# Kernel optimization log

Measured on AMD Instinct MI355X. Metric: run time of the kernel, lower is better.

The kernel has to match this reference:

```python
import jax, jax.numpy as jnp
import numpy as np

B, C, H, W = 8, 256, 128, 128


def _bilinear_sample(img, gx, gy):
    """F.grid_sample(bilinear, padding_mode='zeros', align_corners=False).
    img: [B,C,H,W]; gx, gy: [B,H,W] normalized coords in [-1,1].
    Returns [B,C,H,W]."""
    Bi, Ci, Hi, Wi = img.shape
    ix = ((gx + 1.0) * Wi - 1.0) * 0.5  # pixel x coord
    iy = ((gy + 1.0) * Hi - 1.0) * 0.5  # pixel y coord
    ix0 = jnp.floor(ix)
    iy0 = jnp.floor(iy)
    wx1 = ix - ix0
    wy1 = iy - iy0
    bidx = jnp.arange(Bi)[:, None, None]

    def gather(iyf, ixf):
        valid = (ixf >= 0) & (ixf < Wi) & (iyf >= 0) & (iyf < Hi)
        iyc = jnp.clip(iyf, 0, Hi - 1).astype(jnp.int32)
        ixc = jnp.clip(ixf, 0, Wi - 1).astype(jnp.int32)
        v = img[bidx, :, iyc, ixc]  # [B,H,W,C]
        return jnp.where(valid[..., None], v, jnp.zeros((), img.dtype))

    v00 = gather(iy0, ix0)
    v01 = gather(iy0, ix0 + 1)
    v10 = gather(iy0 + 1, ix0)
    v11 = gather(iy0 + 1, ix0 + 1)
    w00 = ((1.0 - wy1) * (1.0 - wx1))[..., None]
    w01 = ((1.0 - wy1) * wx1)[..., None]
    w10 = (wy1 * (1.0 - wx1))[..., None]
    w11 = (wy1 * wx1)[..., None]
    out = v00 * w00 + v01 * w01 + v10 * w10 + v11 * w11  # [B,H,W,C]
    return out.transpose(0, 3, 1, 2)


def setup_inputs() -> dict:
    key = jax.random.key(0)
    ks = jax.random.split(key, 7)
    s = 1.0 / np.sqrt(C)
    return {
        "x": jax.random.normal(ks[0], (B, C, H, W), jnp.float32),
        "w_dw": jax.random.normal(ks[1], (C,), jnp.float32) * s,        # depthwise 1x1, no bias
        "w_off": jax.random.normal(ks[2], (2, C), jnp.float32) * s,     # offset 1x1 conv C->2
        "b_off": jax.random.normal(ks[3], (2,), jnp.float32) * 0.1,
        "w_pc": jax.random.normal(ks[4], (C, C), jnp.float32) * s,      # pointwise 1x1, no bias
        "w_W": jax.random.normal(ks[5], (C, C), jnp.float32) * s,       # residual-merge 1x1 conv
        "b_W": jax.random.normal(ks[6], (C,), jnp.float32) * 0.1,
    }


def reference(x, w_dw, w_off, b_off, w_pc, w_W, b_W):
    # offset = tanh(Conv1x1(x)) -> one shared (dx, dy) field (group == inplanes)
    offset = jnp.tanh(jnp.einsum('oc,bchw->bohw', w_off, x) + b_off[None, :, None, None])
    # depthwise 1x1 conv (bias=False) == per-channel scale
    dw = x * w_dw[None, :, None, None]
    # base normalized grid: X varies along W, Y along H (np.meshgrid convention)
    gx_base = jnp.linspace(-1.0, 1.0, W)[None, None, :]  # [1,1,W]
    gy_base = jnp.linspace(-1.0, 1.0, H)[None, :, None]  # [1,H,1]
    gx = jnp.clip(gx_base + offset[:, 0], -1.0, 1.0)  # [B,H,W]
    gy = jnp.clip(gy_base + offset[:, 1], -1.0, 1.0)
    sampled = _bilinear_sample(dw, gx, gy)             # [B,C,H,W]
    out = jnp.einsum('oc,bchw->bohw', w_pc, sampled)   # pointwise conv
    out = jnp.einsum('oc,bchw->bohw', w_W, out) + b_W[None, :, None, None]
    return out + x
```

## Files before the change

### kernel.cpp

```cpp
#include <hip/hip_runtime.h>
#include <hip/hip_bf16.h>

#define Bn 8
#define Cn 256
#define Hn 128
#define Wn 128
#define HWn (Hn * Wn)

typedef __attribute__((ext_vector_type(8))) short bfrag8;
typedef __attribute__((ext_vector_type(8))) unsigned short u16x8;
typedef __attribute__((ext_vector_type(4))) float f32x4;
typedef __attribute__((ext_vector_type(4))) unsigned int u32x4;

__device__ __forceinline__ float bf2f(unsigned short u) {
    unsigned int v = ((unsigned int)u) << 16;
    return __builtin_bit_cast(float, v);
}
__device__ __forceinline__ unsigned short f2bf(float f) {
    unsigned int u = __builtin_bit_cast(unsigned int, f);
    unsigned int lsb = (u >> 16) & 1u;
    u += 0x7fffu + lsb;
    return (unsigned short)(u >> 16);
}

__device__ __forceinline__ void load_lds16(const void* g, void* l) {
    __builtin_amdgcn_global_load_lds(
        (const __attribute__((address_space(1))) unsigned int*)g,
        (__attribute__((address_space(3))) unsigned int*)l,
        16, 0, 0);
}

__global__ __launch_bounds__(256)
void build_wcomb(const float* __restrict__ w_dw,
                 const float* __restrict__ w_pc,
                 const float* __restrict__ w_W,
                 unsigned short* __restrict__ wfrag) {
    const int o = blockIdx.x;
    const int c = threadIdx.x;
    float acc = 0.f;
#pragma unroll 8
    for (int k = 0; k < Cn; ++k)
        acc = fmaf(w_W[o * Cn + k], w_pc[k * Cn + c], acc);
    const int ob = o >> 4, lr = o & 15;
    const int ks = c >> 5, lg = (c & 31) >> 3, e = c & 7;
    const int lane = (lg << 4) + lr;
    wfrag[((((ob << 3) + ks) << 6) + lane) * 8 + e] = f2bf(acc * w_dw[c]);
}

__global__ __launch_bounds__(256)
void prep_kernel(const float* __restrict__ x,
                 const float* __restrict__ w_off,
                 const float* __restrict__ b_off,
                 unsigned short* __restrict__ x_t,
                 float2* __restrict__ coords) {
    __shared__ __align__(16) char tile[64 * 512];
    __shared__ float partial[4][64][2];
    const int t = threadIdx.x;
    const int lane = t & 63;
    const int wv = t >> 6;
    int blk = blockIdx.x;
    blk = ((blk & 7) << 8) | (blk >> 3);
    const int b = blk >> 8;
    const int p0 = (blk & 255) << 6;
    const float* xp = x + ((size_t)b * Cn) * HWn + p0;

    float s0 = 0.f, s1 = 0.f;
#pragma unroll 8
    for (int i = 0; i < 64; ++i) {
        int c = (wv << 6) + i;
        float v = xp[(size_t)c * HWn + lane];
        s0 = fmaf(v, w_off[c], s0);
        s1 = fmaf(v, w_off[Cn + c], s1);
        int byte = (lane << 9) + (((c << 1)) ^ ((lane & 7) << 4));
        *reinterpret_cast<unsigned short*>(tile + byte) = f2bf(v);
    }
    partial[wv][lane][0] = s0;
    partial[wv][lane][1] = s1;
    __syncthreads();

    if (t < 64) {
        float o0 = partial[0][t][0] + partial[1][t][0] + partial[2][t][0] + partial[3][t][0] + b_off[0];
        float o1 = partial[0][t][1] + partial[1][t][1] + partial[2][t][1] + partial[3][t][1] + b_off[1];
        o0 = tanhf(o0);
        o1 = tanhf(o1);
        int p = p0 + t;
        int yy = p >> 7, xx = p & 127;
        float gx = fminf(fmaxf(-1.f + xx * (2.f / 127.f) + o0, -1.f), 1.f);
        float gy = fminf(fmaxf(-1.f + yy * (2.f / 127.f) + o1, -1.f), 1.f);
        coords[(size_t)b * HWn + p] = make_float2(gx * 64.f + 63.5f, gy * 64.f + 63.5f);
    }

    const int pp = t >> 2, cc = t & 3;
    unsigned short* dst = x_t + ((size_t)(b * HWn + p0 + pp)) * Cn + (cc << 6);
#pragma unroll
    for (int j = 0; j < 8; ++j) {
        int c2 = ((cc << 6) + (j << 3)) << 1;
        int byte = (pp << 9) + (c2 ^ ((pp & 7) << 4));
        *reinterpret_cast<u32x4*>(dst + (j << 3)) = *reinterpret_cast<const u32x4*>(tile + byte);
    }
}

__global__ __launch_bounds__(512, 2)
void main_kernel(const float* __restrict__ x,
                 const float* __restrict__ b_W,
                 const unsigned short* __restrict__ x_t,
                 const float2* __restrict__ coords,
                 const unsigned short* __restrict__ wfrag,
                 float* __restrict__ out) {
    __shared__ __align__(16) char As[4][32 * 512];
    __shared__ __align__(16) float4 wts[32];
    const int t = threadIdx.x;
    const int lane = t & 63;
    const int wid = t >> 6;
    int blk = blockIdx.x;
    blk = ((blk & 7) << 9) | (blk >> 3);
    const int b = blk >> 9;
    const int p0 = (blk & 511) << 5;
    const size_t pixbase = (size_t)b * HWn + p0;
    const unsigned short* xtb = x_t + (size_t)b * HWn * Cn;

    if (t < 32) {
        float2 co = coords[pixbase + t];
        float ix = co.x, iy = co.y;
        float fx = floorf(ix), fy = floorf(iy);
        int ix0 = (int)fx, iy0 = (int)fy;
        float wx1 = ix - fx, wy1 = iy - fy;
        float wx0 = 1.f - wx1, wy0 = 1.f - wy1;
        bool vx0 = (ix0 >= 0) && (ix0 < Wn);
        bool vx1 = (ix0 >= -1) && (ix0 < Wn - 1);
        bool vy0 = (iy0 >= 0) && (iy0 < Hn);
        bool vy1 = (iy0 >= -1) && (iy0 < Hn - 1);
        float4 w;
        w.x = (vy0 && vx0) ? wy0 * wx0 : 0.f;
        w.y = (vy0 && vx1) ? wy0 * wx1 : 0.f;
        w.z = (vy1 && vx0) ? wy1 * wx0 : 0.f;
        w.w = (vy1 && vx1) ? wy1 * wx1 : 0.f;
        wts[t] = w;
    }

    {
        const int hp = lane >> 5;
        const int j = lane & 31;
        float2 co[2];
#pragma unroll
        for (int i = 0; i < 2; ++i)
            co[i] = coords[pixbase + (wid << 2) + (i << 1) + hp];

#pragma unroll
        for (int i = 0; i < 2; ++i) {
            const int p = (wid << 2) + (i << 1);
            const int px = p + hp;
            float ix = co[i].x, iy = co[i].y;
            int ix0 = (int)floorf(ix), iy0 = (int)floorf(iy);
            int cx0 = min(max(ix0, 0), Wn - 1), cx1 = min(max(ix0 + 1, 0), Wn - 1);
            int cy0 = min(max(iy0, 0), Hn - 1), cy1 = min(max(iy0 + 1, 0), Hn - 1);
            const int gch = (j ^ (px & 15)) << 3;
            const unsigned short* s00 = xtb + (size_t)(cy0 * Wn + cx0) * Cn + gch;
            const unsigned short* s01 = xtb + (size_t)(cy0 * Wn + cx1) * Cn + gch;
            const unsigned short* s10 = xtb + (size_t)(cy1 * Wn + cx0) * Cn + gch;
            const unsigned short* s11 = xtb + (size_t)(cy1 * Wn + cx1) * Cn + gch;
            load_lds16(s00, &As[0][p << 9]);
            load_lds16(s01, &As[1][p << 9]);
            load_lds16(s10, &As[2][p << 9]);
            load_lds16(s11, &As[3][p << 9]);
        }
    }
    __syncthreads();

    {
        const int px = t >> 4;
        const float4 w = wts[px];
#pragma unroll
        for (int q = 0; q < 2; ++q) {
            const int kc = (t & 15) + (q << 4);
            const int off = (px << 9) + ((kc ^ (px & 15)) << 4);
            u16x8 c00 = *reinterpret_cast<const u16x8*>(&As[0][off]);
            u16x8 c01 = *reinterpret_cast<const u16x8*>(&As[1][off]);
            u16x8 c10 = *reinterpret_cast<const u16x8*>(&As[2][off]);
            u16x8 c11 = *reinterpret_cast<const u16x8*>(&As[3][off]);
            u16x8 res;
#pragma unroll
            for (int e = 0; e < 8; ++e) {
                float r = w.x * bf2f(c00[e]) + w.y * bf2f(c01[e])
                        + w.z * bf2f(c10[e]) + w.w * bf2f(c11[e]);
                res[e] = f2bf(r);
            }
            *reinterpret_cast<u16x8*>(&As[0][off]) = res;
        }
    }
    __syncthreads();

    const int lr = lane & 15;
    const int lg = lane >> 4;
    f32x4 acc[2][2];
#pragma unroll
    for (int m = 0; m < 2; ++m)
#pragma unroll
        for (int n = 0; n < 2; ++n)
            acc[m][n] = (f32x4){0.f, 0.f, 0.f, 0.f};

#pragma unroll
    for (int ks = 0; ks < 8; ++ks) {
        bfrag8 a[2], bb[2];
        const int kc = (ks << 2) + lg;
#pragma unroll
        for (int n = 0; n < 2; ++n) {
            const int pr = (n << 4) + lr;
            const int off = (pr << 9) + ((kc ^ (pr & 15)) << 4);
            bb[n] = *reinterpret_cast<const bfrag8*>(&As[0][off]);
        }
#pragma unroll
        for (int m = 0; m < 2; ++m) {
            const int ob = (wid << 1) + m;
            const unsigned short* src = wfrag + ((((ob << 3) + ks) << 6) + lane) * 8;
            a[m] = *reinterpret_cast<const bfrag8*>(src);
        }
#pragma unroll
        for (int m = 0; m < 2; ++m)
#pragma unroll
            for (int n = 0; n < 2; ++n)
                acc[m][n] = __builtin_amdgcn_mfma_f32_16x16x32_bf16(a[m], bb[n], acc[m][n], 0, 0, 0);
    }

#pragma unroll
    for (int m = 0; m < 2; ++m) {
#pragma unroll
        for (int r = 0; r < 4; ++r) {
            int o = (wid << 5) + (m << 4) + (lg << 2) + r;
            float bw = b_W[o];
            size_t rowbase = ((size_t)b * Cn + o) * HWn + p0;
#pragma unroll
            for (int n = 0; n < 2; ++n) {
                size_t idx = rowbase + (n << 4) + lr;
                __builtin_nontemporal_store(acc[m][n][r] + bw + x[idx], &out[idx]);
            }
        }
    }
}

extern "C" void kernel_launch(void* const* d_in, const int* in_sizes, int n_in,
                              void* d_out, int out_size, void* d_ws, size_t ws_size,
                              hipStream_t stream) {
    const float* x     = (const float*)d_in[0];
    const float* w_dw  = (const float*)d_in[1];
    const float* w_off = (const float*)d_in[2];
    const float* b_off = (const float*)d_in[3];
    const float* w_pc  = (const float*)d_in[4];
    const float* w_W   = (const float*)d_in[5];
    const float* b_W   = (const float*)d_in[6];
    float* out = (float*)d_out;

    char* ws = (char*)d_ws;
    unsigned short* x_t   = (unsigned short*)ws;
    float2* coords        = (float2*)(ws + 67108864);
    unsigned short* wcomb = (unsigned short*)(ws + 67108864 + 1048576);

    build_wcomb<<<dim3(256), dim3(256), 0, stream>>>(w_dw, w_pc, w_W, wcomb);
    prep_kernel<<<dim3(2048), dim3(256), 0, stream>>>(x, w_off, b_off, x_t, coords);
    main_kernel<<<dim3(4096), dim3(512), 0, stream>>>(x, b_W, x_t, coords, wcomb, out);
}
```

Measured before the change: 119.0 us.

## Rewrite prep kernel with direct global-to-LDS fp32 loads and 512 threads

The prep kernel now stages the fp32 input tile into shared memory with 16-byte direct global-to-LDS loads, using an XOR swizzle to avoid bank conflicts. It replaces the earlier per-element scalar loads and bf16 stores. Each thread then reads 32 channels for one pixel and computes the offset dot products, with partial sums reduced across lanes by shuffles. It packs the values to bf16 and writes 64-byte rows of the channel-last copy. The block grows to 512 threads and 64 KB of LDS, which may limit how many blocks fit per CU.

```diff
diff --git a/kernel.cpp b/kernel.cpp
--- a/kernel.cpp
+++ b/kernel.cpp
@@ -47,14 +47,14 @@
     wfrag[((((ob << 3) + ks) << 6) + lane) * 8 + e] = f2bf(acc * w_dw[c]);
 }
 
-__global__ __launch_bounds__(256)
+__global__ __launch_bounds__(512, 2)
 void prep_kernel(const float* __restrict__ x,
                  const float* __restrict__ w_off,
                  const float* __restrict__ b_off,
                  unsigned short* __restrict__ x_t,
                  float2* __restrict__ coords) {
-    __shared__ __align__(16) char tile[64 * 512];
-    __shared__ float partial[4][64][2];
+    __shared__ __align__(16) char tile[256 * 256];
+    __shared__ float wo[2][8][33];
     const int t = threadIdx.x;
     const int lane = t & 63;
     const int wv = t >> 6;
@@ -64,39 +64,57 @@
     const int p0 = (blk & 255) << 6;
     const float* xp = x + ((size_t)b * Cn) * HWn + p0;
 
-    float s0 = 0.f, s1 = 0.f;
-#pragma unroll 8
-    for (int i = 0; i < 64; ++i) {
-        int c = (wv << 6) + i;
-        float v = xp[(size_t)c * HWn + lane];
-        s0 = fmaf(v, w_off[c], s0);
-        s1 = fmaf(v, w_off[Cn + c], s1);
-        int byte = (lane << 9) + (((c << 1)) ^ ((lane & 7) << 4));
-        *reinterpret_cast<unsigned short*>(tile + byte) = f2bf(v);
-    }
-    partial[wv][lane][0] = s0;
-    partial[wv][lane][1] = s1;
+    {
+        const int which = t >> 8, c = t & 255;
+        wo[which][c >> 5][c & 31] = w_off[(which << 8) + c];
+    }
+
+    {
+        const int r = lane >> 4;
+        const int q = lane & 15;
+#pragma unroll
+        for (int i = 0; i < 8; ++i) {
+            const int cbase = (wv << 5) + (i << 2);
+            const int c = cbase + r;
+            const int swz = (c ^ (c >> 4)) & 15;
+            const float* src = xp + (size_t)c * HWn + ((q ^ swz) << 2);
+            load_lds16(src, tile + (cbase << 8));
+        }
+    }
     __syncthreads();
 
-    if (t < 64) {
-        float o0 = partial[0][t][0] + partial[1][t][0] + partial[2][t][0] + partial[3][t][0] + b_off[0];
-        float o1 = partial[0][t][1] + partial[1][t][1] + partial[2][t][1] + partial[3][t][1] + b_off[1];
-        o0 = tanhf(o0);
-        o1 = tanhf(o1);
-        int p = p0 + t;
-        int yy = p >> 7, xx = p & 127;
-        float gx = fminf(fmaxf(-1.f + xx * (2.f / 127.f) + o0, -1.f), 1.f);
-        float gy = fminf(fmaxf(-1.f + yy * (2.f / 127.f) + o1, -1.f), 1.f);
-        coords[(size_t)b * HWn + p] = make_float2(gx * 64.f + 63.5f, gy * 64.f + 63.5f);
-    }
-
-    const int pp = t >> 2, cc = t & 3;
-    unsigned short* dst = x_t + ((size_t)(b * HWn + p0 + pp)) * Cn + (cc << 6);
-#pragma unroll
-    for (int j = 0; j < 8; ++j) {
-        int c2 = ((cc << 6) + (j << 3)) << 1;
-        int byte = (pp << 9) + (c2 ^ ((pp & 7) << 4));
-        *reinterpret_cast<u32x4*>(dst + (j << 3)) = *reinterpret_cast<const u32x4*>(tile + byte);
+    {
+        const int pp = t >> 3;
+        const int g = t & 7;
+        float s0 = 0.f, s1 = 0.f;
+        u16x8 res[4];
+#pragma unroll
+        for (int s = 0; s < 32; ++s) {
+            const int c = (g << 5) + s;
+            const int swz = (c ^ (c >> 4)) & 15;
+            const int byte = (c << 8) + ((((pp >> 2) ^ swz)) << 4) + ((pp & 3) << 2);
+            float v = *reinterpret_cast<const float*>(tile + byte);
+            s0 = fmaf(v, wo[0][g][s], s0);
+            s1 = fmaf(v, wo[1][g][s], s1);
+            res[s >> 3][s & 7] = f2bf(v);
+        }
+
+        s0 += __shfl_xor(s0, 1); s0 += __shfl_xor(s0, 2); s0 += __shfl_xor(s0, 4);
+        s1 += __shfl_xor(s1, 1); s1 += __shfl_xor(s1, 2); s1 += __shfl_xor(s1, 4);
+        if (g == 0) {
+            float o0 = tanhf(s0 + b_off[0]);
+            float o1 = tanhf(s1 + b_off[1]);
+            int p = p0 + pp;
+            int yy = p >> 7, xx = p & 127;
+            float gx = fminf(fmaxf(-1.f + xx * (2.f / 127.f) + o0, -1.f), 1.f);
+            float gy = fminf(fmaxf(-1.f + yy * (2.f / 127.f) + o1, -1.f), 1.f);
+            coords[(size_t)b * HWn + p] = make_float2(gx * 64.f + 63.5f, gy * 64.f + 63.5f);
+        }
+
+        unsigned short* dst = x_t + ((size_t)(b * HWn + p0 + pp)) * Cn + (g << 5);
+#pragma unroll
+        for (int j = 0; j < 4; ++j)
+            *reinterpret_cast<u32x4*>(dst + (j << 3)) = __builtin_bit_cast(u32x4, res[j]);
     }
 }
 
@@ -256,6 +274,6 @@
     unsigned short* wcomb = (unsigned short*)(ws + 67108864 + 1048576);
 
     build_wcomb<<<dim3(256), dim3(256), 0, stream>>>(w_dw, w_pc, w_W, wcomb);
-    prep_kernel<<<dim3(2048), dim3(256), 0, stream>>>(x, w_off, b_off, x_t, coords);
+    prep_kernel<<<dim3(2048), dim3(512), 0, stream>>>(x, w_off, b_off, x_t, coords);
     main_kernel<<<dim3(4096), dim3(512), 0, stream>>>(x, b_W, x_t, coords, wcomb, out);
 }
```

Measured after the change: 121.3 us. About the same (+2.0%).
